# Performance work log

Hardware: AMD Instinct MI355X
Metric: run time of the kernel (lower is better)

Reference implementation:

```python
import jax, jax.numpy as jnp
import numpy as np

D_IN = 1024
D_STATE = 1024
B = 128
L = 512


def _linear(x, W, b):
    # torch nn.Linear convention: W is (out, in)
    return x @ W.T + b


def setup_inputs() -> dict:
    key = jax.random.key(0)
    ks = jax.random.split(key, 11)
    s = 0.02
    past = jax.random.normal(ks[0], (B, L, D_IN), dtype=jnp.float32)
    # init_proj: Linear(d_in, d_state) -> SiLU -> Linear(d_state, d_state)
    Wi1 = jax.random.normal(ks[1], (D_STATE, D_IN), jnp.float32) * s
    bi1 = jnp.zeros((D_STATE,), jnp.float32)
    Wi2 = jax.random.normal(ks[2], (D_STATE, D_STATE), jnp.float32) * s
    bi2 = jnp.zeros((D_STATE,), jnp.float32)
    # transition: Linear(d_state+d_in, 2*d_state) -> SiLU -> Linear(2*d_state, d_state) -> SiLU -> Linear(d_state, d_state)
    Wt1 = jax.random.normal(ks[3], (2 * D_STATE, D_STATE + D_IN), jnp.float32) * s
    bt1 = jnp.zeros((2 * D_STATE,), jnp.float32)
    Wt2 = jax.random.normal(ks[4], (D_STATE, 2 * D_STATE), jnp.float32) * s
    bt2 = jnp.zeros((D_STATE,), jnp.float32)
    Wt3 = jax.random.normal(ks[5], (D_STATE, D_STATE), jnp.float32) * s
    bt3 = jnp.zeros((D_STATE,), jnp.float32)
    return {
        "past": past,
        "Wi1": Wi1, "bi1": bi1, "Wi2": Wi2, "bi2": bi2,
        "Wt1": Wt1, "bt1": bt1, "Wt2": Wt2, "bt2": bt2,
        "Wt3": Wt3, "bt3": bt3,
    }


def reference(past, Wi1, bi1, Wi2, bi2, Wt1, bt1, Wt2, bt2, Wt3, bt3):
    # s0 = init_proj(past[:, 0, :])
    h0 = jax.nn.silu(_linear(past[:, 0, :], Wi1, bi1))
    s0 = _linear(h0, Wi2, bi2)  # (B, d_state)

    def step(s_prev, x_t):
        h = jnp.concatenate([s_prev, x_t], axis=-1)  # (B, d_state + d_in)
        h = jax.nn.silu(_linear(h, Wt1, bt1))        # (B, 2*d_state)
        h = jax.nn.silu(_linear(h, Wt2, bt2))        # (B, d_state)
        s = _linear(h, Wt3, bt3)                     # (B, d_state)
        return s, s

    xs = jnp.swapaxes(past[:, 1:, :], 0, 1)          # (L-1, B, d_in)
    _, states_rest = jax.lax.scan(step, s0, xs)      # (L-1, B, d_state)
    states = jnp.concatenate([s0[None], states_rest], axis=0)  # (L, B, d_state)
    return jnp.swapaxes(states, 0, 1)                # (B, L, d_state)
```

## Files before the change

kernel.cpp:

```cpp
#include <hip/hip_runtime.h>
#include <hip/hip_bf16.h>


typedef __bf16 v8bf __attribute__((ext_vector_type(8)));
typedef float f32x4 __attribute__((ext_vector_type(4)));
typedef unsigned u32x4 __attribute__((ext_vector_type(4)));

#define REP1 (128 * 2048)
#define REP2 (128 * 1024)

__device__ inline f32x4 mfma16(v8bf a, v8bf b, f32x4 c) {
  return __builtin_amdgcn_mfma_f32_16x16x32_bf16(a, b, c, 0, 0, 0);
}
__device__ inline float silu_f(float x) { return x / (1.f + __expf(-x)); }
__device__ inline v8bf as8(f32x4 x) { union { f32x4 f; v8bf b; } u; u.f = x; return u.b; }
__device__ inline v8bf cvt8(float4 a, float4 b) {
  v8bf v;
  v[0] = (__bf16)a.x; v[1] = (__bf16)a.y; v[2] = (__bf16)a.z; v[3] = (__bf16)a.w;
  v[4] = (__bf16)b.x; v[5] = (__bf16)b.y; v[6] = (__bf16)b.z; v[7] = (__bf16)b.w;
  return v;
}
__device__ inline unsigned bfb(float v) {
  __bf16 b = (__bf16)v; unsigned short u; __builtin_memcpy(&u, &b, 2); return (unsigned)u;
}

#define CLOADP(dst, base, boff)                                        \
  asm volatile("global_load_dwordx4 %0, %1, off offset:%2"             \
               : "=v"(dst) : "v"(base), "n"(boff))
#define CLOADC(dst, base)                                              \
  asm volatile("global_load_dwordx4 %0, %1, off sc0 sc1" : "=v"(dst) : "v"(base))

template <int N> __device__ inline void vwait() {
  asm volatile("s_waitcnt vmcnt(%0)" :: "n"(N) : "memory");
  __builtin_amdgcn_sched_barrier(0);
}
__device__ inline void vwait_n(int n) {
  switch (n) {
    case 0: vwait<0>(); break;   case 1: vwait<1>(); break;
    case 2: vwait<2>(); break;   case 3: vwait<3>(); break;
    case 4: vwait<4>(); break;   case 5: vwait<5>(); break;
    case 6: vwait<6>(); break;   case 7: vwait<7>(); break;
    case 8: vwait<8>(); break;   case 9: vwait<9>(); break;
    case 10: vwait<10>(); break; case 11: vwait<11>(); break;
    case 12: vwait<12>(); break; case 13: vwait<13>(); break;
    case 14: vwait<14>(); break; default: vwait<15>(); break;
  }
}

__device__ inline void poll32(const unsigned* f, unsigned tgt, int* dead) {
  if (threadIdx.x < 8 && !*dead) {
    const unsigned* p = f + threadIdx.x * 4;
    int guard = 0;
    while (true) {
      u32x4 v;
      asm volatile("global_load_dwordx4 %0, %1, off sc0 sc1\n\ts_waitcnt vmcnt(0)"
                   : "=v"(v) : "v"(p) : "memory");
      if (v[0] >= tgt && v[1] >= tgt && v[2] >= tgt && v[3] >= tgt) break;
      if (++guard > (1 << 18)) { *dead = 1; break; }
      __builtin_amdgcn_s_sleep(1);
    }
  }
  __syncthreads();
}
__device__ inline void release(unsigned* f, int slot, unsigned v) {
  asm volatile("s_waitcnt vmcnt(0)" ::: "memory");
  __syncthreads();
  if (threadIdx.x == 0)
    asm volatile("global_store_dword %0, %1, off sc0 sc1" :: "v"(f + slot), "v"(v) : "memory");
}

__global__ void cvt_kernel(const float* __restrict__ src, __bf16* __restrict__ dst,
                           int total8, int log2cols, int sstride, int soff) {
  int i = blockIdx.x * 256 + threadIdx.x;
  if (i >= total8) return;
  long long e = (long long)i * 8;
  int r = (int)(e >> log2cols);
  int c = (int)(e & ((1LL << log2cols) - 1));
  const float* s = src + (size_t)r * sstride + soff + c;
  float4 f0 = *(const float4*)(s);
  float4 f1 = *(const float4*)(s + 4);
  *(v8bf*)(dst + e) = cvt8(f0, f1);
}

__global__ void tpose_kernel(const float* __restrict__ src, __bf16* __restrict__ dst,
                             int R, int C) {
  __shared__ float tile[32][33];
  const int tid = threadIdx.x;
  const int r0 = blockIdx.y * 32, c0 = blockIdx.x * 32;
  const int lr = tid >> 5, lc = tid & 31;
#pragma unroll
  for (int p = 0; p < 4; ++p)
    tile[lr + p * 8][lc] = src[(size_t)(r0 + lr + p * 8) * C + c0 + lc];
  __syncthreads();
#pragma unroll
  for (int p = 0; p < 4; ++p)
    dst[(size_t)(c0 + lr + p * 8) * R + r0 + lc] = (__bf16)tile[lc][lr + p * 8];
}

__global__ __launch_bounds__(256, 1) void comp_gemm_kernel(
    const __bf16* __restrict__ A, const __bf16* __restrict__ B,
    __bf16* __restrict__ out) {
  const int tid = threadIdx.x, wid = tid >> 6, lane = tid & 63;
  const int lr = lane & 15, lc = lane >> 4;
  const int m0 = blockIdx.x * 32;
  const int c0 = blockIdx.y * 128 + wid * 32;
  const __bf16* ap0 = A + (size_t)(m0 + lr) * 1024 + lc * 8;
  const __bf16* ap1 = ap0 + (size_t)16 * 1024;
  const __bf16* bp = B + (size_t)(c0 + lr) * 1024 + lc * 8;
  f32x4 acc[2][2] = {};
#pragma unroll 8
  for (int k = 0; k < 1024; k += 32) {
    v8bf a0 = *(const v8bf*)(ap0 + k);
    v8bf a1 = *(const v8bf*)(ap1 + k);
#pragma unroll
    for (int f = 0; f < 2; ++f) {
      v8bf b = *(const v8bf*)(bp + (size_t)f * 16 * 1024 + k);
      acc[0][f] = mfma16(a0, b, acc[0][f]);
      acc[1][f] = mfma16(a1, b, acc[1][f]);
    }
  }
  const int cm = lc << 2, cn = lr;
#pragma unroll
  for (int mf = 0; mf < 2; ++mf)
#pragma unroll
    for (int f = 0; f < 2; ++f)
#pragma unroll
      for (int r = 0; r < 4; ++r)
        out[(size_t)(m0 + mf * 16 + cm + r) * 1024 + c0 + f * 16 + cn] =
            (__bf16)acc[mf][f][r];
}

__global__ void bias_comp_kernel(const float* __restrict__ Wt1,
                                 const float* __restrict__ bt3,
                                 const float* __restrict__ bi2,
                                 float* __restrict__ b13, float* __restrict__ b1i2) {
  const int n = blockIdx.x * 4 + (threadIdx.x >> 6);
  const int lane = threadIdx.x & 63;
  const float* row = Wt1 + (size_t)n * 2048;
  float v1 = 0.f, v2 = 0.f;
#pragma unroll
  for (int i = 0; i < 16; ++i) {
    int k = lane + i * 64;
    float w = row[k];
    v1 += w * bt3[k];
    v2 += w * bi2[k];
  }
  for (int o = 32; o; o >>= 1) { v1 += __shfl_down(v1, o); v2 += __shfl_down(v2, o); }
  if (lane == 0) { b13[n] = v1; b1i2[n] = v2; }
}

template <bool BF16A>
__global__ __launch_bounds__(512, 1) void xc_gemm_kernel(
    const void* __restrict__ pastv, const __bf16* __restrict__ w1x,
    const float* __restrict__ bt1, __bf16* __restrict__ xc) {
  const int t = blockIdx.z + 1;
  const int mh = blockIdx.y;
  const int nb = blockIdx.x;
  const int tid = threadIdx.x, wid = tid >> 6, lane = tid & 63;
  const int wm = wid >> 2, wn = wid & 3;
  const int m0 = mh * 64 + wm * 32;
  const int n0 = nb * 512 + wn * 128;
  const int lr = lane & 15, lc = lane >> 4;
  f32x4 acc[2][8] = {};
  const __bf16* bp = w1x + (size_t)(n0 + lr) * 1024 + lc * 8;
  if constexpr (BF16A) {
    const __bf16* a0p = (const __bf16*)pastv +
                        ((size_t)(m0 + lr) * 512 + t) * 1024 + lc * 8;
    const __bf16* a1p = a0p + (size_t)16 * 512 * 1024;
#pragma unroll 4
    for (int k = 0; k < 1024; k += 32) {
      v8bf a0 = *(const v8bf*)(a0p + k);
      v8bf a1 = *(const v8bf*)(a1p + k);
#pragma unroll
      for (int j = 0; j < 8; ++j) {
        v8bf b = *(const v8bf*)(bp + (size_t)j * 16 * 1024 + k);
        acc[0][j] = mfma16(a0, b, acc[0][j]);
        acc[1][j] = mfma16(a1, b, acc[1][j]);
      }
    }
  } else {
    const float* a0p = (const float*)pastv +
                       ((size_t)(m0 + lr) * 512 + t) * 1024 + lc * 8;
    const float* a1p = a0p + (size_t)16 * 512 * 1024;
#pragma unroll 4
    for (int k = 0; k < 1024; k += 32) {
      float4 x00 = *(const float4*)(a0p + k);
      float4 x01 = *(const float4*)(a0p + k + 4);
      float4 x10 = *(const float4*)(a1p + k);
      float4 x11 = *(const float4*)(a1p + k + 4);
      v8bf a0 = cvt8(x00, x01), a1 = cvt8(x10, x11);
#pragma unroll
      for (int j = 0; j < 8; ++j) {
        v8bf b = *(const v8bf*)(bp + (size_t)j * 16 * 1024 + k);
        acc[0][j] = mfma16(a0, b, acc[0][j]);
        acc[1][j] = mfma16(a1, b, acc[1][j]);
      }
    }
  }
  const int cm = lc << 2, cn = lr;
#pragma unroll
  for (int f = 0; f < 2; ++f)
#pragma unroll
    for (int j = 0; j < 8; ++j) {
      int n = n0 + j * 16 + cn;
      float bias = bt1[n];
#pragma unroll
      for (int r = 0; r < 4; ++r) {
        int m = m0 + f * 16 + cm + r;
        xc[((size_t)m * 512 + t) * 2048 + n] = (__bf16)(acc[f][j][r] + bias);
      }
    }
}

template <int K>
__device__ inline void stage_issue(f32x4* v, const __bf16* src, int tid) {
  constexpr int KC = K / 8;
#pragma unroll
  for (int i = 0; i < K / 128; ++i) {
    int idx = tid + i * 256;
    int row = idx / KC, kc = idx % KC;
    CLOADC(v[i], src + (size_t)row * K + kc * 8);
  }
}
template <int K>
__device__ inline void stage_commit(char* lds, f32x4* v, int tid) {
  constexpr int KC = K / 8;
#pragma unroll
  for (int i = 0; i < K / 128; ++i) {
    int idx = tid + i * 256;
    int row = idx / KC, kc = idx % KC;
    unsigned byte = ((unsigned)(row * K + kc * 8) * 2) ^ ((unsigned)(row & 7) << 4);
    *(f32x4*)(lds + byte) = v[i];
  }
  __syncthreads();
}

template <int KIT, int PFD, int KSB>
__device__ inline f32x4 ring_run1(const char* ldsa, int k0, const __bf16* wtb,
                                  f32x4 (&rw)[PFD], int lane) {
  const int lr = lane & 15, lc = lane >> 4;
  f32x4 acc = {0.f, 0.f, 0.f, 0.f};
#pragma unroll
  for (int it = 0; it < KIT; ++it) {
    vwait_n((KIT - 1 - it) < (PFD - 1) ? (KIT - 1 - it) : (PFD - 1));
    v8bf b = as8(rw[it % PFD]);
    if (it + PFD < KIT) CLOADP(rw[it % PFD], wtb, (it + PFD) * 64);
    int k = k0 + it * 32 + lc * 8;
    unsigned byte = ((unsigned)(lr * KSB + k) * 2) ^ ((unsigned)(lr & 7) << 4);
    v8bf a = *(const v8bf*)(ldsa + byte);
    acc = mfma16(a, b, acc);
  }
  return acc;
}
template <int PFD>
__device__ inline void ring_pre(const __bf16* wtb, f32x4 (&rw)[PFD]) {
#pragma unroll
  for (int j = 0; j < PFD; ++j) CLOADP(rw[j], wtb, j * 64);
}

__device__ inline f32x4 gemm_aa16(const char* ldsa, int k0, const char* ldsw,
                                  int kb0, int col, int lane) {
  const int lr = lane & 15, lc = lane >> 4;
  f32x4 acc = {0.f, 0.f, 0.f, 0.f};
#pragma unroll
  for (int it = 0; it < 16; ++it) {
    int k = k0 + it * 32 + lc * 8;
    unsigned abyte = ((unsigned)(lr * 1024 + k) * 2) ^ ((unsigned)(lr & 7) << 4);
    v8bf a = *(const v8bf*)(ldsa + abyte);
    v8bf b = *(const v8bf*)(ldsw + (size_t)((kb0 + it * 4 + lc) * 32 + col) * 16);
    acc = mfma16(a, b, acc);
  }
  return acc;
}

__global__ __launch_bounds__(256, 1) void recurrent_kernel(
    const __bf16* __restrict__ wWi1, const __bf16* __restrict__ wWi2,
    const __bf16* __restrict__ wW13, const __bf16* __restrict__ wW1i2,
    const __bf16* __restrict__ wWt2, const __bf16* __restrict__ wWt3,
    const __bf16* __restrict__ x0bf,
    __bf16* __restrict__ z1, __bf16* __restrict__ z2,
    const float* __restrict__ bi1, const float* __restrict__ bi2,
    const float* __restrict__ bt2, const float* __restrict__ bt3,
    const float* __restrict__ b13, const float* __restrict__ b1i2,
    float* __restrict__ out, unsigned* __restrict__ flags) {
  __shared__ alignas(16) char actbuf[65536];
  __shared__ alignas(16) char wt3buf[65536];
  __shared__ alignas(16) char scratch[4096];
  __shared__ int s_dead;
  const int bid = blockIdx.x;
  const int g = bid >> 5, s = bid & 31;
  const int tid = threadIdx.x, wid = tid >> 6, lane = tid & 63;
  const int lr = lane & 15, lc = lane >> 4;
  const int cm = lc << 2, cn = lr;
  const int wn = wid & 1, wk = wid >> 1;
  const int b0 = g * 16;
  if (tid == 0) s_dead = 0;

  unsigned* fA = flags + g * 64;
  unsigned* fB = fA + 32;
  const __bf16* xc = (const __bf16*)out;
  __bf16* tposeb = (__bf16*)scratch;
  float* red = (float*)scratch;
  float* fin = (float*)(scratch + 2048);

  {
    const __bf16* wg = wWt3 + (size_t)s * 32 * 1024;
    for (int idx = tid; idx < 4096; idx += 256) {
      int kb = idx >> 5, c = idx & 31;
      *(f32x4*)(wt3buf + (size_t)idx * 16) = *(const f32x4*)(wg + (size_t)c * 1024 + kb * 8);
    }
  }

  const int nBC = s * 32 + wn * 16 + cn;
  const int nA = s * 64 + wid * 16 + cn;
  const float bB = bt2[nBC], bCt = bt3[nBC];
  const float bI1 = bi1[nBC], bC0 = bi2[nBC];
  const float bA13 = b13[nA], bA1i2 = b1i2[nA];

  auto storeZ2 = [&](__bf16* base) {
    int row = tid >> 4, col = (tid * 2) & 31;
    unsigned d = bfb(fin[row * 32 + col]) | (bfb(fin[row * 32 + col + 1]) << 16);
    __bf16* p = base + (size_t)(b0 + row) * 1024 + s * 32 + col;
    asm volatile("global_store_dword %0, %1, off sc0 sc1" :: "v"(p), "v"(d) : "memory");
  };
  auto storeOut = [&](int tt) {
    int row = tid >> 4, col = (tid * 2) & 31;
    float2 o; o.x = fin[row * 32 + col]; o.y = fin[row * 32 + col + 1];
    *(float2*)(out + (size_t)(b0 + row) * 524288 + (size_t)tt * 1024 + s * 32 + col) = o;
  };

  {
    f32x4 sv[8];
    stage_issue<1024>(sv, x0bf + (size_t)b0 * 1024, tid);
    f32x4 rw[8];
    const __bf16* wtb = wWi1 + (size_t)(nBC - cn + lr) * 1024 + wk * 512 + lc * 8;
    ring_pre<8>(wtb, rw);
    vwait<0>();
    stage_commit<1024>(actbuf, sv, tid);
    f32x4 acc = ring_run1<16, 8, 1024>(actbuf, wk * 512, wtb, rw, lane);
    if (wk) {
#pragma unroll
      for (int r = 0; r < 4; ++r) red[wn * 256 + (cm + r) * 16 + cn] = acc[r];
    }
    __syncthreads();
    if (!wk) {
#pragma unroll
      for (int r = 0; r < 4; ++r)
        fin[(cm + r) * 32 + wn * 16 + cn] =
            silu_f(acc[r] + red[wn * 256 + (cm + r) * 16 + cn] + bI1);
    }
    __syncthreads();
    storeZ2(z2);
    release(fB, s, 1u);
  }

  for (int t = 1; t < 512; ++t) {
    {
      const __bf16* wtbA = (t == 1 ? wW1i2 : wW13) +
                           (size_t)(s * 64 + wid * 16 + lr) * 1024 + lc * 8;
      const float bAv = (t == 1) ? bA1i2 : bA13;
      unsigned xcu[4];
#pragma unroll
      for (int r = 0; r < 4; ++r) {
        const __bf16* p = xc + ((size_t)(b0 + cm + r) * 512 + t) * 2048 + nA;
        asm volatile("global_load_ushort %0, %1, off sc0 sc1" : "=v"(xcu[r]) : "v"(p));
      }
      f32x4 rw[16];
      ring_pre<16>(wtbA, rw);
      poll32(fB, (unsigned)t, &s_dead);
      f32x4 sv[8];
      stage_issue<1024>(sv, z2 + (size_t)((t - 1) & 1) * REP2 + (size_t)b0 * 1024, tid);
      vwait<0>();
      stage_commit<1024>(actbuf, sv, tid);
      f32x4 acc = ring_run1<32, 16, 1024>(actbuf, 0, wtbA, rw, lane);
#pragma unroll
      for (int r = 0; r < 4; ++r) {
        float xv = __uint_as_float(xcu[r] << 16);
        tposeb[(cm + r) * 64 + wid * 16 + cn] = (__bf16)silu_f(acc[r] + xv + bAv);
      }
      __syncthreads();
      {
        int row = tid >> 4, col = (tid * 4) & 63;
        unsigned long long d = *(const unsigned long long*)(tposeb + row * 64 + col);
        __bf16* p = z1 + (size_t)(b0 + row) * 2048 + s * 64 + col;
        asm volatile("global_store_dwordx2 %0, %1, off sc0 sc1" :: "v"(p), "v"(d) : "memory");
      }
      release(fA, s, (unsigned)t);
    }
    {
      f32x4 acc;
      if (t == 1) {
        const __bf16* wtbC = wWi2 + (size_t)(nBC - cn + lr) * 1024 + wk * 512 + lc * 8;
        f32x4 rw[8];
        ring_pre<8>(wtbC, rw);
        acc = ring_run1<16, 8, 1024>(actbuf, wk * 512, wtbC, rw, lane);
      } else {
        acc = gemm_aa16(actbuf, wk * 512, wt3buf, wk * 64, wn * 16 + lr, lane);
      }
      const float bCv = (t == 1) ? bC0 : bCt;
      if (wk) {
#pragma unroll
        for (int r = 0; r < 4; ++r) red[wn * 256 + (cm + r) * 16 + cn] = acc[r];
      }
      __syncthreads();
      if (!wk) {
#pragma unroll
        for (int r = 0; r < 4; ++r)
          fin[(cm + r) * 32 + wn * 16 + cn] =
              acc[r] + red[wn * 256 + (cm + r) * 16 + cn] + bCv;
      }
      __syncthreads();
      storeOut(t - 1);
    }
    {
      const __bf16* wtbB = wWt2 + (size_t)(nBC - cn + lr) * 2048 + wk * 1024 + lc * 8;
      f32x4 rw[16];
      ring_pre<16>(wtbB, rw);
      poll32(fA, (unsigned)t, &s_dead);
      f32x4 sv[16];
      stage_issue<2048>(sv, z1 + (size_t)b0 * 2048, tid);
      vwait<0>();
      stage_commit<2048>(actbuf, sv, tid);
      f32x4 acc = ring_run1<32, 16, 2048>(actbuf, wk * 1024, wtbB, rw, lane);
      if (wk) {
#pragma unroll
        for (int r = 0; r < 4; ++r) red[wn * 256 + (cm + r) * 16 + cn] = acc[r];
      }
      __syncthreads();
      if (!wk) {
#pragma unroll
        for (int r = 0; r < 4; ++r)
          fin[(cm + r) * 32 + wn * 16 + cn] =
              silu_f(acc[r] + red[wn * 256 + (cm + r) * 16 + cn] + bB);
      }
      __syncthreads();
      storeZ2(z2 + (size_t)(t & 1) * REP2);
      release(fB, s, (unsigned)(t + 1));
    }
  }
  {
    poll32(fB, 512u, &s_dead);
    f32x4 sv[8];
    stage_issue<1024>(sv, z2 + (size_t)1 * REP2 + (size_t)b0 * 1024, tid);
    vwait<0>();
    stage_commit<1024>(actbuf, sv, tid);
    f32x4 acc = gemm_aa16(actbuf, wk * 512, wt3buf, wk * 64, wn * 16 + lr, lane);
    if (wk) {
#pragma unroll
      for (int r = 0; r < 4; ++r) red[wn * 256 + (cm + r) * 16 + cn] = acc[r];
    }
    __syncthreads();
    if (!wk) {
#pragma unroll
      for (int r = 0; r < 4; ++r)
        fin[(cm + r) * 32 + wn * 16 + cn] =
            acc[r] + red[wn * 256 + (cm + r) * 16 + cn] + bCt;
    }
    __syncthreads();
    storeOut(511);
  }
}

extern "C" void kernel_launch(void* const* d_in, const int* in_sizes, int n_in,
                              void* d_out, int out_size, void* d_ws, size_t ws_size,
                              hipStream_t stream) {
  (void)in_sizes; (void)n_in; (void)out_size;
  const float* past = (const float*)d_in[0];
  const float* Wi1 = (const float*)d_in[1];
  const float* bi1 = (const float*)d_in[2];
  const float* Wi2 = (const float*)d_in[3];
  const float* bi2 = (const float*)d_in[4];
  const float* Wt1 = (const float*)d_in[5];
  const float* bt1 = (const float*)d_in[6];
  const float* Wt2 = (const float*)d_in[7];
  const float* bt2 = (const float*)d_in[8];
  const float* Wt3 = (const float*)d_in[9];
  const float* bt3 = (const float*)d_in[10];
  float* out = (float*)d_out;

  char* ws = (char*)d_ws;
  size_t off = 0;
  unsigned* flags = (unsigned*)(ws + off); off += 4096;
  __bf16* wWi1 = (__bf16*)(ws + off);  off += (size_t)1024 * 1024 * 2;
  __bf16* wWi2 = (__bf16*)(ws + off);  off += (size_t)1024 * 1024 * 2;
  __bf16* wWt1s = (__bf16*)(ws + off); off += (size_t)2048 * 1024 * 2;
  __bf16* wWt1x = (__bf16*)(ws + off); off += (size_t)2048 * 1024 * 2;
  __bf16* wWt2 = (__bf16*)(ws + off);  off += (size_t)1024 * 2048 * 2;
  __bf16* wWt3 = (__bf16*)(ws + off);  off += (size_t)1024 * 1024 * 2;
  __bf16* wWt3T = (__bf16*)(ws + off); off += (size_t)1024 * 1024 * 2;
  __bf16* wWi2T = (__bf16*)(ws + off); off += (size_t)1024 * 1024 * 2;
  __bf16* wW13 = (__bf16*)(ws + off);  off += (size_t)2048 * 1024 * 2;
  __bf16* wW1i2 = (__bf16*)(ws + off); off += (size_t)2048 * 1024 * 2;
  float* b13 = (float*)(ws + off);     off += 2048 * 4;
  float* b1i2 = (float*)(ws + off);    off += 2048 * 4;
  __bf16* x0bf = (__bf16*)(ws + off);  off += (size_t)128 * 1024 * 2;
  __bf16* z1 = (__bf16*)(ws + off);    off += (size_t)REP1 * 2;
  __bf16* z2 = (__bf16*)(ws + off);    off += (size_t)2 * REP2 * 2;
  __bf16* pbf = (__bf16*)(ws + off);
  const size_t need_pbf = off + (size_t)128 * 512 * 1024 * 2;
  const bool use_pbf = ws_size >= need_pbf;

  hipMemsetAsync(flags, 0, 4096, stream);

  auto cvt = [&](const float* s, __bf16* d, size_t rows, int cols, int log2c,
                 int sstride, int soff) {
    int total8 = (int)(rows * (size_t)cols / 8);
    cvt_kernel<<<dim3((total8 + 255) / 256), dim3(256), 0, stream>>>(
        s, d, total8, log2c, sstride, soff);
  };
  cvt(Wi1, wWi1, 1024, 1024, 10, 1024, 0);
  cvt(Wi2, wWi2, 1024, 1024, 10, 1024, 0);
  cvt(Wt1, wWt1s, 2048, 1024, 10, 2048, 0);
  cvt(Wt1, wWt1x, 2048, 1024, 10, 2048, 1024);
  cvt(Wt2, wWt2, 1024, 2048, 11, 2048, 0);
  cvt(Wt3, wWt3, 1024, 1024, 10, 1024, 0);
  cvt(past, x0bf, 128, 1024, 10, 512 * 1024, 0);

  tpose_kernel<<<dim3(32, 32), dim3(256), 0, stream>>>(Wt3, wWt3T, 1024, 1024);
  tpose_kernel<<<dim3(32, 32), dim3(256), 0, stream>>>(Wi2, wWi2T, 1024, 1024);
  comp_gemm_kernel<<<dim3(64, 8), dim3(256), 0, stream>>>(wWt1s, wWt3T, wW13);
  comp_gemm_kernel<<<dim3(64, 8), dim3(256), 0, stream>>>(wWt1s, wWi2T, wW1i2);
  bias_comp_kernel<<<dim3(512), dim3(256), 0, stream>>>(Wt1, bt3, bi2, b13, b1i2);

  if (use_pbf) {
    cvt(past, pbf, (size_t)128 * 512, 1024, 10, 1024, 0);
    xc_gemm_kernel<true><<<dim3(4, 2, 511), dim3(512), 0, stream>>>(
        pbf, wWt1x, bt1, (__bf16*)d_out);
  } else {
    xc_gemm_kernel<false><<<dim3(4, 2, 511), dim3(512), 0, stream>>>(
        past, wWt1x, bt1, (__bf16*)d_out);
  }

  recurrent_kernel<<<dim3(256), dim3(256), 0, stream>>>(
      wWi1, wWi2, wW13, wW1i2, wWt2, wWt3, x0bf, z1, z2,
      bi1, bi2, bt2, bt3, b13, b1i2, out, flags);
}
```

Measured before the change: 7.541 ms.

## Poll producer flags in four chunks and issue activation loads per chunk

Splits the single wait on all 32 producer flags into four waits of 8 flags each. After each wait the block issues global loads for the matching quarter of the activation columns, so loading can start as soon as that part of the producers is done instead of after all of them. The cost is four polls plus block-wide barriers where there was one, and a chunked staging layout that has to stay consistent with the LDS swizzle.

After: 8.754 ms. 16.1% more time.

```diff
diff --git a/kernel.cpp b/kernel.cpp
--- a/kernel.cpp
+++ b/kernel.cpp
@@ -49,6 +49,21 @@
 
 __device__ inline void poll32(const unsigned* f, unsigned tgt, int* dead) {
   if (threadIdx.x < 8 && !*dead) {
+    const unsigned* p = f + threadIdx.x * 4;
+    int guard = 0;
+    while (true) {
+      u32x4 v;
+      asm volatile("global_load_dwordx4 %0, %1, off sc0 sc1\n\ts_waitcnt vmcnt(0)"
+                   : "=v"(v) : "v"(p) : "memory");
+      if (v[0] >= tgt && v[1] >= tgt && v[2] >= tgt && v[3] >= tgt) break;
+      if (++guard > (1 << 18)) { *dead = 1; break; }
+      __builtin_amdgcn_s_sleep(1);
+    }
+  }
+  __syncthreads();
+}
+__device__ inline void poll8(const unsigned* f, unsigned tgt, int* dead) {
+  if (threadIdx.x < 2 && !*dead) {
     const unsigned* p = f + threadIdx.x * 4;
     int guard = 0;
     while (true) {
@@ -235,6 +250,34 @@
   __syncthreads();
 }
 
+template <int K>
+__device__ inline void stage_issue_c(f32x4* v, const __bf16* src, int tid, int c) {
+  constexpr int CK8 = K / 32;
+  constexpr int L = (16 * CK8) / 256;
+#pragma unroll
+  for (int j = 0; j < L; ++j) {
+    int idx = tid + j * 256;
+    int row = idx / CK8, kl = idx % CK8;
+    CLOADC(v[c * L + j], src + (size_t)row * K + (size_t)(c * CK8 + kl) * 8);
+  }
+}
+template <int K>
+__device__ inline void stage_commit_all(char* lds, f32x4* v, int tid) {
+  constexpr int CK8 = K / 32;
+  constexpr int L = (16 * CK8) / 256;
+#pragma unroll
+  for (int c = 0; c < 4; ++c)
+#pragma unroll
+    for (int j = 0; j < L; ++j) {
+      int idx = tid + j * 256;
+      int row = idx / CK8, kl = idx % CK8;
+      int kc = c * CK8 + kl;
+      unsigned byte = ((unsigned)(row * K + kc * 8) * 2) ^ ((unsigned)(row & 7) << 4);
+      *(f32x4*)(lds + byte) = v[c * L + j];
+    }
+  __syncthreads();
+}
+
 template <int KIT, int PFD, int KSB>
 __device__ inline f32x4 ring_run1(const char* ldsa, int k0, const __bf16* wtb,
                                   f32x4 (&rw)[PFD], int lane) {
@@ -367,11 +410,15 @@
       }
       f32x4 rw[16];
       ring_pre<16>(wtbA, rw);
-      poll32(fB, (unsigned)t, &s_dead);
+      const __bf16* z2src = z2 + (size_t)((t - 1) & 1) * REP2 + (size_t)b0 * 1024;
       f32x4 sv[8];
-      stage_issue<1024>(sv, z2 + (size_t)((t - 1) & 1) * REP2 + (size_t)b0 * 1024, tid);
+#pragma unroll
+      for (int c = 0; c < 4; ++c) {
+        poll8(fB + c * 8, (unsigned)t, &s_dead);
+        stage_issue_c<1024>(sv, z2src, tid, c);
+      }
       vwait<0>();
-      stage_commit<1024>(actbuf, sv, tid);
+      stage_commit_all<1024>(actbuf, sv, tid);
       f32x4 acc = ring_run1<32, 16, 1024>(actbuf, 0, wtbA, rw, lane);
 #pragma unroll
       for (int r = 0; r < 4; ++r) {
@@ -416,11 +463,15 @@
       const __bf16* wtbB = wWt2 + (size_t)(nBC - cn + lr) * 2048 + wk * 1024 + lc * 8;
       f32x4 rw[16];
       ring_pre<16>(wtbB, rw);
-      poll32(fA, (unsigned)t, &s_dead);
+      const __bf16* z1src = z1 + (size_t)b0 * 2048;
       f32x4 sv[16];
-      stage_issue<2048>(sv, z1 + (size_t)b0 * 2048, tid);
+#pragma unroll
+      for (int c = 0; c < 4; ++c) {
+        poll8(fA + c * 8, (unsigned)t, &s_dead);
+        stage_issue_c<2048>(sv, z1src, tid, c);
+      }
       vwait<0>();
-      stage_commit<2048>(actbuf, sv, tid);
+      stage_commit_all<2048>(actbuf, sv, tid);
       f32x4 acc = ring_run1<32, 16, 2048>(actbuf, wk * 1024, wtbB, rw, lane);
       if (wk) {
 #pragma unroll
```
